# Performance work log

Measured on AMD Instinct MI355X. Metric: run time of the kernel, lower is better.

## Reference

```python
import jax, jax.numpy as jnp
import numpy as np

N, E, H = 50000, 200000, 4
IN, ED = 256, 12
C1, C2 = 256, 64
G, NPG = 100, 500  # 100 graphs x 500 nodes
EPS = 1e-5
SLOPE = 0.2


def gatv2(x, src, dst, edge_attr, Wl, bl, Wr, br, We, att, bias, n_nodes, heads, ch):
    # GATv2Conv (PyG semantics): message j->i, aggregate at target i=edge_index[1]
    xl = (x @ Wl + bl).reshape(n_nodes, heads, ch)   # source transform
    xr = (x @ Wr + br).reshape(n_nodes, heads, ch)   # target transform
    e = (edge_attr @ We).reshape(-1, heads, ch)
    m = xl[src] + xr[dst] + e                        # [E,H,C]
    s = jax.nn.leaky_relu(m, SLOPE)
    logits = jnp.einsum('ehc,hc->eh', s, att)        # [E,H]
    # segment softmax over destination nodes
    mx = jax.ops.segment_max(logits, dst, num_segments=n_nodes)
    ex = jnp.exp(logits - mx[dst])
    den = jax.ops.segment_sum(ex, dst, num_segments=n_nodes)
    alpha = ex / (den[dst] + 1e-16)                  # [E,H]
    out = jax.ops.segment_sum(xl[src] * alpha[:, :, None], dst, num_segments=n_nodes)
    return out.reshape(n_nodes, heads * ch) + bias


def bn_eval(x, gamma, beta, mean, var):
    return (x - mean) * jax.lax.rsqrt(var + EPS) * gamma + beta


def setup_inputs() -> dict:
    key = jax.random.key(0)
    ks = list(jax.random.split(key, 40))
    rn = lambda k, shp, s=0.05: jax.random.normal(k, shp, jnp.float32) * s
    inp = {
        'x': rn(ks[0], (N, IN), 1.0),
        'edge_index': jax.random.randint(ks[1], (2, E), 0, N),
        'edge_attr': rn(ks[2], (E, ED), 1.0),
        'n_nodes': jnp.full((G,), NPG, dtype=jnp.int32),
        # conv1 params (in=IN, out=C1, heads=H)
        'Wl1': rn(ks[3], (IN, H * C1)), 'bl1': rn(ks[4], (H * C1,)),
        'Wr1': rn(ks[5], (IN, H * C1)), 'br1': rn(ks[6], (H * C1,)),
        'We1': rn(ks[7], (ED, H * C1)),
        'att1': rn(ks[8], (H, C1)), 'b1': rn(ks[9], (H * C1,)),
        # bn1 (eval mode running stats)
        'g1': 1.0 + rn(ks[10], (H * C1,)), 'be1': rn(ks[11], (H * C1,)),
        'm1': rn(ks[12], (H * C1,)), 'v1': 1.0 + 0.1 * jax.random.uniform(ks[13], (H * C1,)),
        # conv2 params (in=H*C1, out=C2, heads=H)
        'Wl2': rn(ks[14], (H * C1, H * C2)), 'bl2': rn(ks[15], (H * C2,)),
        'Wr2': rn(ks[16], (H * C1, H * C2)), 'br2': rn(ks[17], (H * C2,)),
        'We2': rn(ks[18], (ED, H * C2)),
        'att2': rn(ks[19], (H, C2)), 'b2': rn(ks[20], (H * C2,)),
        'g2': 1.0 + rn(ks[21], (H * C2,)), 'be2': rn(ks[22], (H * C2,)),
        'm2': rn(ks[23], (H * C2,)), 'v2': 1.0 + 0.1 * jax.random.uniform(ks[24], (H * C2,)),
        # head MLP
        'Wf1': rn(ks[25], (H * C2, 64)), 'bf1': rn(ks[26], (64,)),
        'Wf2': rn(ks[27], (64, 1)), 'bf2': rn(ks[28], (1,)),
    }
    return inp


def reference(x, edge_index, edge_attr, n_nodes,
              Wl1, bl1, Wr1, br1, We1, att1, b1, g1, be1, m1, v1,
              Wl2, bl2, Wr2, br2, We2, att2, b2, g2, be2, m2, v2,
              Wf1, bf1, Wf2, bf2):
    src, dst = edge_index[0], edge_index[1]
    h = gatv2(x, src, dst, edge_attr, Wl1, bl1, Wr1, br1, We1, att1, b1, N, H, C1)
    h = bn_eval(jax.nn.relu(h), g1, be1, m1, v1)
    h = gatv2(h, src, dst, edge_attr, Wl2, bl2, Wr2, br2, We2, att2, b2, N, H, C2)
    h = bn_eval(jax.nn.relu(h), g2, be2, m2, v2)
    last_idx = jnp.cumsum(n_nodes) - 1                # master node per graph
    master = h[last_idx]                              # [G, 256]
    out = jax.nn.relu(master @ Wf1 + bf1) @ Wf2 + bf2  # [G, 1]
    return out
```

## Files before the change

### kernel.cpp

```cpp
#include <hip/hip_runtime.h>
#include <math.h>

#define NN 50000
#define NE 200000
#define NH 4
#define NG 100
#define EPSBN 1e-5f
#define SLOPE 0.2f

typedef __attribute__((ext_vector_type(8))) short bf16x8;
typedef __attribute__((ext_vector_type(4))) float f32x4;

union U8 { bf16x8 v; uint4 q; unsigned w[4]; };

__device__ __forceinline__ unsigned short f2bf(float f) {
    unsigned u = __float_as_uint(f);
    unsigned r = (u + 0x7fffu + ((u >> 16) & 1u)) >> 16;
    return (unsigned short)r;
}
__device__ __forceinline__ float bf2f(unsigned short s) {
    return __uint_as_float(((unsigned)s) << 16);
}

__global__ void fill_val(float* p, int n, float v) {
    int i = blockIdx.x * 256 + threadIdx.x;
    if (i < n) p[i] = v;
}

__global__ void wprep1t(const float* __restrict__ Wl, const float* __restrict__ Wr,
                        unsigned short* __restrict__ Bh) {
    int idx = blockIdx.x * 256 + threadIdx.x;
    int n = idx & 511, k = (idx >> 9) & 255, h = idx >> 17;
    const float* W = (n < 256) ? Wl : Wr;
    float w = W[(size_t)k * 1024 + h * 256 + (n & 255)];
    size_t dst = (size_t)h * 131072 + (((size_t)(n >> 4) * 8 + (k >> 5)) << 9)
               + ((((k >> 3) & 3) << 4) + (n & 15)) * 8 + (k & 7);
    Bh[dst] = f2bf(w);
}
__global__ void wprep2t(const float* __restrict__ Wl, const float* __restrict__ Wr,
                        unsigned short* __restrict__ Bh) {
    int idx = blockIdx.x * 256 + threadIdx.x;
    int n = idx >> 10, k = idx & 1023;
    const float* W = (n < 256) ? Wl : Wr;
    float w = W[(size_t)k * 256 + (n & 255)];
    size_t dst = (((size_t)(n >> 4) * 32 + (k >> 5)) << 9)
               + ((((k >> 3) & 3) << 4) + (n & 15)) * 8 + (k & 7);
    Bh[dst] = f2bf(w);
}

__device__ __forceinline__ void cvt_split(const float4& v0, const float4& v1,
                                          bf16x8& h, bf16x8& l) {
    float vv[8];
    *(float4*)&vv[0] = v0; *(float4*)&vv[4] = v1;
    U8 uh, ul;
#pragma unroll
    for (int j = 0; j < 4; ++j) {
        float a0 = vv[2 * j], a1 = vv[2 * j + 1];
        unsigned u0 = __float_as_uint(a0), u1 = __float_as_uint(a1);
        uh.w[j] = (u0 >> 16) | (u1 & 0xFFFF0000u);
        float l0 = a0 - __uint_as_float(u0 & 0xFFFF0000u);
        float l1 = a1 - __uint_as_float(u1 & 0xFFFF0000u);
        ul.w[j] = (unsigned)f2bf(l0) | ((unsigned)f2bf(l1) << 16);
    }
    h = uh.v; l = ul.v;
}

template<int MODE>
__launch_bounds__(512, 4)
__global__ void gemm_bs(const float* __restrict__ Af,
                        const unsigned short* __restrict__ Atile,
                        const unsigned short* __restrict__ Bh, int KT,
                        const float* __restrict__ bL, const float* __restrict__ bR,
                        unsigned short* __restrict__ C, int M) {
    __shared__ unsigned short Bs[16384];
    const int p = blockIdx.x;
    const int strip = ((p >> 6) << 3) + (p & 7);
    if (strip * 256 >= M) return;
    const int slice = (p >> 3) & 7;
    const int m0 = strip * 256;
    const int tid = threadIdx.x;
    const int lane = tid & 63, w = tid >> 6;
    const int r15 = lane & 15, kq = lane >> 4;
    const size_t sliceBase = (size_t)slice * 4 * KT * 64;

    f32x4 acc[2][4];
#pragma unroll
    for (int m = 0; m < 2; ++m)
#pragma unroll
        for (int n = 0; n < 4; ++n) acc[m][n] = (f32x4){0.f, 0.f, 0.f, 0.f};

    const float* aPtr[2];
    const unsigned short* a2Ptr[2];
#pragma unroll
    for (int m = 0; m < 2; ++m) {
        if (MODE == 0) {
            int row = m0 + w * 32 + m * 16 + r15;
            row = row < M ? row : M - 1;
            aPtr[m] = Af + (size_t)row * 256 + kq * 8;
        } else {
            a2Ptr[m] = Atile + (size_t)(strip * 16 + w * 2 + m) * 16384 + lane * 8;
        }
    }

    float4 curA[2][2];
    bf16x8 curH[2], midH[2];
    if (MODE == 0) {
#pragma unroll
        for (int m = 0; m < 2; ++m) {
            curA[m][0] = *(const float4*)(aPtr[m]);
            curA[m][1] = *(const float4*)(aPtr[m] + 4);
        }
    } else {
#pragma unroll
        for (int m = 0; m < 2; ++m) {
            curH[m] = *(const bf16x8*)(a2Ptr[m]);
            midH[m] = *(const bf16x8*)(a2Ptr[m] + 512);
        }
    }

    const int nchunks = KT / 8;
    for (int kc = 0; kc < nchunks; ++kc) {
        {
            const uint4* gh = (const uint4*)Bh + sliceBase;
            uint4* lh = (uint4*)Bs;
#pragma unroll
            for (int i = 0; i < 4; ++i) {
                int u = i * 512 + tid;
                int nt = u >> 9;
                int ktl = (u & 511) >> 6, j = u & 63;
                lh[u] = gh[((size_t)nt * KT + kc * 8 + ktl) * 64 + j];
            }
        }
        __syncthreads();

#pragma unroll
        for (int ktl = 0; ktl < 8; ++ktl) {
            const int kt = kc * 8 + ktl;
            float4 nxtA[2][2];
            bf16x8 nxtH[2];
            const bool hn1 = (kt + 1 < KT), hn2 = (kt + 2 < KT);
            if (MODE == 0) {
                if (hn1) {
#pragma unroll
                    for (int m = 0; m < 2; ++m) {
                        nxtA[m][0] = *(const float4*)(aPtr[m] + (size_t)(kt + 1) * 32);
                        nxtA[m][1] = *(const float4*)(aPtr[m] + (size_t)(kt + 1) * 32 + 4);
                    }
                }
            } else {
                if (hn2) {
#pragma unroll
                    for (int m = 0; m < 2; ++m)
                        nxtH[m] = *(const bf16x8*)(a2Ptr[m] + (size_t)(kt + 2) * 512);
                }
            }
            bf16x8 ah[2], al[2];
            if (MODE == 0) {
#pragma unroll
                for (int m = 0; m < 2; ++m)
                    cvt_split(curA[m][0], curA[m][1], ah[m], al[m]);
            } else {
#pragma unroll
                for (int m = 0; m < 2; ++m) ah[m] = curH[m];
            }
#pragma unroll
            for (int n = 0; n < 4; ++n) {
                bf16x8 bh = *(const bf16x8*)&Bs[(n * 8 + ktl) * 512 + lane * 8];
#pragma unroll
                for (int m = 0; m < 2; ++m) {
                    acc[m][n] = __builtin_amdgcn_mfma_f32_16x16x32_bf16(
                        ah[m], bh, acc[m][n], 0, 0, 0);
                    if (MODE == 0)
                        acc[m][n] = __builtin_amdgcn_mfma_f32_16x16x32_bf16(
                            al[m], bh, acc[m][n], 0, 0, 0);
                }
            }
            if (MODE == 0) {
                if (hn1) {
#pragma unroll
                    for (int m = 0; m < 2; ++m) {
                        curA[m][0] = nxtA[m][0];
                        curA[m][1] = nxtA[m][1];
                    }
                }
            } else {
#pragma unroll
                for (int m = 0; m < 2; ++m) {
                    curH[m] = midH[m];
                    if (hn2) midH[m] = nxtH[m];
                }
            }
        }
        __syncthreads();
    }
#pragma unroll
    for (int n = 0; n < 4; ++n) {
        int gcol = slice * 64 + n * 16 + r15;
        float bv = (gcol < 256) ? bL[gcol] : bR[gcol - 256];
#pragma unroll
        for (int m = 0; m < 2; ++m) {
#pragma unroll
            for (int r = 0; r < 4; ++r) {
                int grow = m0 + w * 32 + m * 16 + kq * 4 + r;
                if (grow < M)
                    C[(size_t)grow * 512 + gcol] = f2bf(acc[m][n][r] + bv);
            }
        }
    }
}

#define SCAN_BLOCKS 196

__global__ void csr_count(const int* __restrict__ ei, int* __restrict__ cnt) {
    int e = blockIdx.x * 256 + threadIdx.x;
    if (e < NE) atomicAdd(&cnt[ei[NE + e]], 1);
}
__global__ void csr_bsum(const int* __restrict__ cnt, int* __restrict__ bsum) {
    __shared__ int s[256];
    int idx = blockIdx.x * 256 + threadIdx.x;
    int v = idx < NN ? cnt[idx] : 0;
    s[threadIdx.x] = v;
    __syncthreads();
    for (int d = 128; d > 0; d >>= 1) {
        if (threadIdx.x < d) s[threadIdx.x] += s[threadIdx.x + d];
        __syncthreads();
    }
    if (threadIdx.x == 0) bsum[blockIdx.x] = s[0];
}
__global__ void csr_scan_bsum(int* __restrict__ bsum) {
    __shared__ int s[256];
    int t = threadIdx.x;
    int v = t < SCAN_BLOCKS ? bsum[t] : 0;
    s[t] = v;
    __syncthreads();
    for (int d = 1; d < 256; d <<= 1) {
        int x = (t >= d) ? s[t - d] : 0;
        __syncthreads();
        s[t] += x;
        __syncthreads();
    }
    if (t < SCAN_BLOCKS) bsum[t] = s[t] - v;
}
__global__ void csr_apply(const int* __restrict__ cnt, const int* __restrict__ bsum,
                          int* __restrict__ off, int* __restrict__ cursor) {
    __shared__ int s[256];
    int idx = blockIdx.x * 256 + threadIdx.x;
    int v = (idx < NN) ? cnt[idx] : 0;
    s[threadIdx.x] = v;
    __syncthreads();
    for (int d = 1; d < 256; d <<= 1) {
        int x = (threadIdx.x >= d) ? s[threadIdx.x - d] : 0;
        __syncthreads();
        s[threadIdx.x] += x;
        __syncthreads();
    }
    int o = bsum[blockIdx.x] + s[threadIdx.x] - v;
    if (idx < NN) { off[idx] = o; cursor[idx] = o; }
    if (idx == NN - 1) off[NN] = o + v;
}
__global__ void csr_fill(const int* __restrict__ ei, int* __restrict__ cursor,
                         int* __restrict__ eidl) {
    int e = blockIdx.x * 256 + threadIdx.x;
    if (e < NE) {
        int d = ei[NE + e];
        int p = atomicAdd(&cursor[d], 1);
        eidl[p] = e;
    }
}

__device__ __forceinline__ float edge_part(const float4& l, const float4& r,
                                           const float* ev, const float (*rW)[4],
                                           const float4& attv) {
    const float* lp = &l.x; const float* rp = &r.x; const float* ap = &attv.x;
    float part = 0.f;
#pragma unroll
    for (int j = 0; j < 4; ++j) {
        float ecf = 0.f;
#pragma unroll
        for (int d = 0; d < 12; ++d) ecf = fmaf(ev[d], rW[d][j], ecf);
        float mv = lp[j] + rp[j] + ecf;
        mv = mv > 0.f ? mv : SLOPE * mv;
        part = fmaf(mv, ap[j], part);
    }
    return part;
}

template<int NHEADS, int OUTMODE>
__launch_bounds__(256)
__global__ void node_fused(const unsigned short* __restrict__ x16,
                           const int* __restrict__ off, const int* __restrict__ eidl,
                           const int* __restrict__ ei, const float* __restrict__ ea,
                           const float* __restrict__ We, int ldwe,
                           const float* __restrict__ att,
                           const float* __restrict__ bias, const float* __restrict__ gam,
                           const float* __restrict__ bet, const float* __restrict__ mu,
                           const float* __restrict__ var,
                           unsigned short* __restrict__ h1t, int hcol,
                           float* __restrict__ fout) {
    const int n = blockIdx.x * 4 + (threadIdx.x >> 6);
    const int lane = threadIdx.x & 63;
    const int cf = lane * 4;
    float rW[12][4];
#pragma unroll
    for (int d = 0; d < 12; ++d) {
        float4 w = *(const float4*)&We[(size_t)d * ldwe + cf];
        rW[d][0] = w.x; rW[d][1] = w.y; rW[d][2] = w.z; rW[d][3] = w.w;
    }
    const float4 attv = *(const float4*)&att[cf];
    float4 xr4;
    {
        ushort4 u = *(const ushort4*)(x16 + (size_t)n * 512 + 256 + cf);
        xr4 = make_float4(bf2f(u.x), bf2f(u.y), bf2f(u.z), bf2f(u.w));
    }
    float acc[4] = {0.f, 0.f, 0.f, 0.f};
    float den = 0.f;
    const int beg = off[n], end = off[n + 1];
    constexpr int RED = 64 / NHEADS;
    int k = beg;
    for (; k + 2 <= end; k += 2) {
        int e0 = eidl[k], e1 = eidl[k + 1];
        int s0 = ei[e0], s1 = ei[e1];
        float ev0[12], ev1[12];
        const float2* p0 = (const float2*)(ea + (size_t)e0 * 12);
        const float2* p1 = (const float2*)(ea + (size_t)e1 * 12);
#pragma unroll
        for (int d = 0; d < 6; ++d) {
            float2 a = p0[d], b = p1[d];
            ev0[2 * d] = a.x; ev0[2 * d + 1] = a.y;
            ev1[2 * d] = b.x; ev1[2 * d + 1] = b.y;
        }
        ushort4 u0 = *(const ushort4*)(x16 + (size_t)s0 * 512 + cf);
        ushort4 u1 = *(const ushort4*)(x16 + (size_t)s1 * 512 + cf);
        float4 l0 = make_float4(bf2f(u0.x), bf2f(u0.y), bf2f(u0.z), bf2f(u0.w));
        float4 l1 = make_float4(bf2f(u1.x), bf2f(u1.y), bf2f(u1.z), bf2f(u1.w));
        float pa = edge_part(l0, xr4, ev0, rW, attv);
        float pb = edge_part(l1, xr4, ev1, rW, attv);
#pragma unroll
        for (int o = RED / 2; o > 0; o >>= 1) {
            pa += __shfl_xor(pa, o);
            pb += __shfl_xor(pb, o);
        }
        float ex0 = __expf(pa), ex1 = __expf(pb);
        den += ex0 + ex1;
        const float* lp0 = &l0.x; const float* lp1 = &l1.x;
#pragma unroll
        for (int j = 0; j < 4; ++j)
            acc[j] = fmaf(ex0, lp0[j], fmaf(ex1, lp1[j], acc[j]));
    }
    if (k < end) {
        int e0 = eidl[k];
        int s0 = ei[e0];
        float ev0[12];
        const float2* p0 = (const float2*)(ea + (size_t)e0 * 12);
#pragma unroll
        for (int d = 0; d < 6; ++d) {
            float2 a = p0[d];
            ev0[2 * d] = a.x; ev0[2 * d + 1] = a.y;
        }
        ushort4 u0 = *(const ushort4*)(x16 + (size_t)s0 * 512 + cf);
        float4 l0 = make_float4(bf2f(u0.x), bf2f(u0.y), bf2f(u0.z), bf2f(u0.w));
        float pa = edge_part(l0, xr4, ev0, rW, attv);
#pragma unroll
        for (int o = RED / 2; o > 0; o >>= 1) pa += __shfl_xor(pa, o);
        float ex0 = __expf(pa);
        den += ex0;
        const float* lp0 = &l0.x;
#pragma unroll
        for (int j = 0; j < 4; ++j) acc[j] = fmaf(ex0, lp0[j], acc[j]);
    }
    const float inv = 1.f / (den + 1e-16f);
    float o[4];
#pragma unroll
    for (int j = 0; j < 4; ++j) {
        int c = cf + j;
        float t = fmaxf(acc[j] * inv + bias[c], 0.f);
        o[j] = (t - mu[c]) * rsqrtf(var[c] + EPSBN) * gam[c] + bet[c];
    }
    if (OUTMODE == 0) {
        ushort4 hv;
        hv.x = f2bf(o[0]); hv.y = f2bf(o[1]); hv.z = f2bf(o[2]); hv.w = f2bf(o[3]);
        const int kt = (hcol >> 5) + (cf >> 5);
        size_t idx = (size_t)(n >> 4) * 16384 + (size_t)kt * 512
                   + ((((cf >> 3) & 3) << 4) + (n & 15)) * 8 + (cf & 7);
        *(ushort4*)(h1t + idx) = hv;
    } else {
        *(float4*)(fout + (size_t)n * 256 + cf) = make_float4(o[0], o[1], o[2], o[3]);
    }
}

__launch_bounds__(64)
__global__ void head_mlp(const float* __restrict__ h2, const int* __restrict__ n_nodes,
                         const float* __restrict__ Wf1, const float* __restrict__ bf1,
                         const float* __restrict__ Wf2, const float* __restrict__ bf2,
                         float* __restrict__ out) {
    const int g = blockIdx.x;
    const int t = threadIdx.x;
    int acc = 0;
    for (int i = t; i <= g; i += 64) acc += n_nodes[i];
#pragma unroll
    for (int off = 32; off > 0; off >>= 1) acc += __shfl_xor(acc, off);
    const int node = acc - 1;
    __shared__ float row[256];
    for (int i = t; i < 256; i += 64) row[i] = h2[(size_t)node * 256 + i];
    __syncthreads();
    float hid = bf1[t];
    for (int k = 0; k < 256; ++k) hid = fmaf(row[k], Wf1[k * 64 + t], hid);
    hid = fmaxf(hid, 0.f);
    float p = hid * Wf2[t];
#pragma unroll
    for (int off = 32; off > 0; off >>= 1) p += __shfl_xor(p, off);
    if (t == 0) out[g] = p + bf2[0];
}

extern "C" void kernel_launch(void* const* d_in, const int* in_sizes, int n_in,
                              void* d_out, int out_size, void* d_ws, size_t ws_size,
                              hipStream_t stream) {
    const float* x   = (const float*)d_in[0];
    const int*   ei  = (const int*)d_in[1];
    const float* ea  = (const float*)d_in[2];
    const int*   nnd = (const int*)d_in[3];
    const float* Wl1 = (const float*)d_in[4];
    const float* bl1 = (const float*)d_in[5];
    const float* Wr1 = (const float*)d_in[6];
    const float* br1 = (const float*)d_in[7];
    const float* We1 = (const float*)d_in[8];
    const float* att1= (const float*)d_in[9];
    const float* b1  = (const float*)d_in[10];
    const float* g1  = (const float*)d_in[11];
    const float* be1 = (const float*)d_in[12];
    const float* m1  = (const float*)d_in[13];
    const float* v1  = (const float*)d_in[14];
    const float* Wl2 = (const float*)d_in[15];
    const float* bl2 = (const float*)d_in[16];
    const float* Wr2 = (const float*)d_in[17];
    const float* br2 = (const float*)d_in[18];
    const float* We2 = (const float*)d_in[19];
    const float* att2= (const float*)d_in[20];
    const float* b2  = (const float*)d_in[21];
    const float* g2  = (const float*)d_in[22];
    const float* be2 = (const float*)d_in[23];
    const float* m2  = (const float*)d_in[24];
    const float* v2  = (const float*)d_in[25];
    const float* Wf1 = (const float*)d_in[26];
    const float* bf1 = (const float*)d_in[27];
    const float* Wf2 = (const float*)d_in[28];
    const float* bf2 = (const float*)d_in[29];
    float* out = (float*)d_out;

    const size_t XB = (size_t)NN * 512 * 2;
    const size_t HB = (size_t)3136 * 16384 * 2;
    const size_t WPB = (size_t)524288 * 2;
    char* ws = (char*)d_ws;
    size_t off = 0;
    unsigned short* panel = (unsigned short*)(ws + off); off += XB;
    unsigned short* h1t   = (unsigned short*)(ws + off);
    float*          h2f   = (float*)(ws + off);    off += HB;
    unsigned short* B1h = (unsigned short*)(ws + off); off += WPB;
    unsigned short* B2h = (unsigned short*)(ws + off); off += WPB;
    int* cnt    = (int*)(ws + off); off += (size_t)NN * 4;
    int* csroff = (int*)(ws + off); off += ((size_t)(NN + 1) * 4 + 15) & ~15ull;
    int* cursor = (int*)(ws + off); off += (size_t)NN * 4;
    int* eidl   = (int*)(ws + off); off += (size_t)NE * 4;
    int* bsum   = (int*)(ws + off); off += ((size_t)SCAN_BLOCKS * 4 + 15) & ~15ull;
    if (ws_size < off) {
        fill_val<<<(out_size + 255) / 256, 256, 0, stream>>>(out, out_size, 1e30f);
        return;
    }

    hipMemsetAsync(cnt, 0, (size_t)NN * 4, stream);
    csr_count<<<(NE + 255) / 256, 256, 0, stream>>>(ei, cnt);
    csr_bsum<<<SCAN_BLOCKS, 256, 0, stream>>>(cnt, bsum);
    csr_scan_bsum<<<1, 256, 0, stream>>>(bsum);
    csr_apply<<<SCAN_BLOCKS, 256, 0, stream>>>(cnt, bsum, csroff, cursor);
    csr_fill<<<(NE + 255) / 256, 256, 0, stream>>>(ei, cursor, eidl);

    wprep1t<<<2048, 256, 0, stream>>>(Wl1, Wr1, B1h);
    wprep2t<<<2048, 256, 0, stream>>>(Wl2, Wr2, B2h);

    const int gemmBlocks = 25 * 64;
    const int nodeBlocks = NN / 4;

    for (int h = 0; h < NH; ++h) {
        gemm_bs<0><<<gemmBlocks, 512, 0, stream>>>(
            x, nullptr, B1h + (size_t)h * 131072, 8,
            bl1 + h * 256, br1 + h * 256, panel, NN);
        node_fused<1, 0><<<nodeBlocks, 256, 0, stream>>>(
            panel, csroff, eidl, ei, ea, We1 + h * 256, 1024, att1 + h * 256,
            b1 + h * 256, g1 + h * 256, be1 + h * 256, m1 + h * 256, v1 + h * 256,
            h1t, h * 256, nullptr);
    }

    gemm_bs<1><<<gemmBlocks, 512, 0, stream>>>(
        nullptr, h1t, B2h, 32, bl2, br2, panel, NN);
    node_fused<4, 1><<<nodeBlocks, 256, 0, stream>>>(
        panel, csroff, eidl, ei, ea, We2, 256, att2, b2, g2, be2, m2, v2,
        nullptr, 0, h2f);

    head_mlp<<<NG, 64, 0, stream>>>(h2f, nnd, Wf1, bf1, Wf2, bf2, out);
}
```

Measured before the change: 830.5 us.

## Pre-convert input features to tiled bf16 once, drop split-precision layer-1 GEMM

Adds an xprep kernel that converts x to bf16 once, in the MFMA tile layout, and zero-pads it to a multiple of 16 rows. All four per-head layer-1 GEMMs then use the same bf16-tile path as layer 2. This removes the per-head fp32 reads, the per-tile hi/lo split and the second MFMA for the low part. It also drops the hi/lo split on x, which lowers layer-1 precision and may push results past tolerance.

New measurement: 704.0 us. 15.2% less time.

```diff
diff --git a/kernel.cpp b/kernel.cpp
--- a/kernel.cpp
+++ b/kernel.cpp
@@ -7,11 +7,10 @@
 #define NG 100
 #define EPSBN 1e-5f
 #define SLOPE 0.2f
+#define NROWT 3128
 
 typedef __attribute__((ext_vector_type(8))) short bf16x8;
 typedef __attribute__((ext_vector_type(4))) float f32x4;
-
-union U8 { bf16x8 v; uint4 q; unsigned w[4]; };
 
 __device__ __forceinline__ unsigned short f2bf(float f) {
     unsigned u = __float_as_uint(f);
@@ -48,30 +47,32 @@
     Bh[dst] = f2bf(w);
 }
 
-__device__ __forceinline__ void cvt_split(const float4& v0, const float4& v1,
-                                          bf16x8& h, bf16x8& l) {
-    float vv[8];
-    *(float4*)&vv[0] = v0; *(float4*)&vv[4] = v1;
-    U8 uh, ul;
-#pragma unroll
-    for (int j = 0; j < 4; ++j) {
-        float a0 = vv[2 * j], a1 = vv[2 * j + 1];
-        unsigned u0 = __float_as_uint(a0), u1 = __float_as_uint(a1);
-        uh.w[j] = (u0 >> 16) | (u1 & 0xFFFF0000u);
-        float l0 = a0 - __uint_as_float(u0 & 0xFFFF0000u);
-        float l1 = a1 - __uint_as_float(u1 & 0xFFFF0000u);
-        ul.w[j] = (unsigned)f2bf(l0) | ((unsigned)f2bf(l1) << 16);
-    }
-    h = uh.v; l = ul.v;
-}
-
-template<int MODE>
+__global__ void xprep(const float* __restrict__ x, unsigned short* __restrict__ xt) {
+    int idx = blockIdx.x * 256 + threadIdx.x;
+    int row = idx >> 5;
+    if (row >= NROWT * 16) return;
+    int k8 = (idx & 31) << 3;
+    unsigned short o[8];
+    if (row < NN) {
+        float4 v0 = *(const float4*)(x + (size_t)row * 256 + k8);
+        float4 v1 = *(const float4*)(x + (size_t)row * 256 + k8 + 4);
+        o[0] = f2bf(v0.x); o[1] = f2bf(v0.y); o[2] = f2bf(v0.z); o[3] = f2bf(v0.w);
+        o[4] = f2bf(v1.x); o[5] = f2bf(v1.y); o[6] = f2bf(v1.z); o[7] = f2bf(v1.w);
+    } else {
+#pragma unroll
+        for (int j = 0; j < 8; ++j) o[j] = 0;
+    }
+    size_t dst = (size_t)(row >> 4) * 4096 + (size_t)(k8 >> 5) * 512
+               + ((((k8 >> 3) & 3) << 4) + (row & 15)) * 8;
+    *(ushort4*)(xt + dst) = *(ushort4*)&o[0];
+    *(ushort4*)(xt + dst + 4) = *(ushort4*)&o[4];
+}
+
 __launch_bounds__(512, 4)
-__global__ void gemm_bs(const float* __restrict__ Af,
-                        const unsigned short* __restrict__ Atile,
-                        const unsigned short* __restrict__ Bh, int KT,
-                        const float* __restrict__ bL, const float* __restrict__ bR,
-                        unsigned short* __restrict__ C, int M) {
+__global__ void gemm_t(const unsigned short* __restrict__ Atile,
+                       const unsigned short* __restrict__ Bh, int KT,
+                       const float* __restrict__ bL, const float* __restrict__ bR,
+                       unsigned short* __restrict__ C, int M) {
     __shared__ unsigned short Bs[16384];
     const int p = blockIdx.x;
     const int strip = ((p >> 6) << 3) + (p & 7);
@@ -82,6 +83,7 @@
     const int lane = tid & 63, w = tid >> 6;
     const int r15 = lane & 15, kq = lane >> 4;
     const size_t sliceBase = (size_t)slice * 4 * KT * 64;
+    const size_t tileStride = (size_t)KT * 512;
 
     f32x4 acc[2][4];
 #pragma unroll
@@ -89,33 +91,16 @@
 #pragma unroll
         for (int n = 0; n < 4; ++n) acc[m][n] = (f32x4){0.f, 0.f, 0.f, 0.f};
 
-    const float* aPtr[2];
-    const unsigned short* a2Ptr[2];
+    const unsigned short* aPtr[2];
+#pragma unroll
+    for (int m = 0; m < 2; ++m)
+        aPtr[m] = Atile + (size_t)(strip * 16 + w * 2 + m) * tileStride + lane * 8;
+
+    bf16x8 curH[2], midH[2];
 #pragma unroll
     for (int m = 0; m < 2; ++m) {
-        if (MODE == 0) {
-            int row = m0 + w * 32 + m * 16 + r15;
-            row = row < M ? row : M - 1;
-            aPtr[m] = Af + (size_t)row * 256 + kq * 8;
-        } else {
-            a2Ptr[m] = Atile + (size_t)(strip * 16 + w * 2 + m) * 16384 + lane * 8;
-        }
-    }
-
-    float4 curA[2][2];
-    bf16x8 curH[2], midH[2];
-    if (MODE == 0) {
-#pragma unroll
-        for (int m = 0; m < 2; ++m) {
-            curA[m][0] = *(const float4*)(aPtr[m]);
-            curA[m][1] = *(const float4*)(aPtr[m] + 4);
-        }
-    } else {
-#pragma unroll
-        for (int m = 0; m < 2; ++m) {
-            curH[m] = *(const bf16x8*)(a2Ptr[m]);
-            midH[m] = *(const bf16x8*)(a2Ptr[m] + 512);
-        }
+        curH[m] = *(const bf16x8*)(aPtr[m]);
+        midH[m] = *(const bf16x8*)(aPtr[m] + 512);
     }
 
     const int nchunks = KT / 8;
@@ -136,59 +121,25 @@
 #pragma unroll
         for (int ktl = 0; ktl < 8; ++ktl) {
             const int kt = kc * 8 + ktl;
-            float4 nxtA[2][2];
             bf16x8 nxtH[2];
-            const bool hn1 = (kt + 1 < KT), hn2 = (kt + 2 < KT);
-            if (MODE == 0) {
-                if (hn1) {
-#pragma unroll
-                    for (int m = 0; m < 2; ++m) {
-                        nxtA[m][0] = *(const float4*)(aPtr[m] + (size_t)(kt + 1) * 32);
-                        nxtA[m][1] = *(const float4*)(aPtr[m] + (size_t)(kt + 1) * 32 + 4);
-                    }
-                }
-            } else {
-                if (hn2) {
-#pragma unroll
-                    for (int m = 0; m < 2; ++m)
-                        nxtH[m] = *(const bf16x8*)(a2Ptr[m] + (size_t)(kt + 2) * 512);
-                }
-            }
-            bf16x8 ah[2], al[2];
-            if (MODE == 0) {
+            const bool hn2 = (kt + 2 < KT);
+            if (hn2) {
 #pragma unroll
                 for (int m = 0; m < 2; ++m)
-                    cvt_split(curA[m][0], curA[m][1], ah[m], al[m]);
-            } else {
-#pragma unroll
-                for (int m = 0; m < 2; ++m) ah[m] = curH[m];
+                    nxtH[m] = *(const bf16x8*)(aPtr[m] + (size_t)(kt + 2) * 512);
             }
 #pragma unroll
             for (int n = 0; n < 4; ++n) {
                 bf16x8 bh = *(const bf16x8*)&Bs[(n * 8 + ktl) * 512 + lane * 8];
 #pragma unroll
-                for (int m = 0; m < 2; ++m) {
+                for (int m = 0; m < 2; ++m)
                     acc[m][n] = __builtin_amdgcn_mfma_f32_16x16x32_bf16(
-                        ah[m], bh, acc[m][n], 0, 0, 0);
-                    if (MODE == 0)
-                        acc[m][n] = __builtin_amdgcn_mfma_f32_16x16x32_bf16(
-                            al[m], bh, acc[m][n], 0, 0, 0);
-                }
+                        curH[m], bh, acc[m][n], 0, 0, 0);
             }
-            if (MODE == 0) {
-                if (hn1) {
-#pragma unroll
-                    for (int m = 0; m < 2; ++m) {
-                        curA[m][0] = nxtA[m][0];
-                        curA[m][1] = nxtA[m][1];
-                    }
-                }
-            } else {
-#pragma unroll
-                for (int m = 0; m < 2; ++m) {
-                    curH[m] = midH[m];
-                    if (hn2) midH[m] = nxtH[m];
-                }
+#pragma unroll
+            for (int m = 0; m < 2; ++m) {
+                curH[m] = midH[m];
+                if (hn2) midH[m] = nxtH[m];
             }
         }
         __syncthreads();
@@ -449,12 +400,14 @@
 
     const size_t XB = (size_t)NN * 512 * 2;
     const size_t HB = (size_t)3136 * 16384 * 2;
+    const size_t XTB = (size_t)NROWT * 4096 * 2;
     const size_t WPB = (size_t)524288 * 2;
     char* ws = (char*)d_ws;
     size_t off = 0;
     unsigned short* panel = (unsigned short*)(ws + off); off += XB;
     unsigned short* h1t   = (unsigned short*)(ws + off);
     float*          h2f   = (float*)(ws + off);    off += HB;
+    unsigned short* xt    = (unsigned short*)(ws + off); off += XTB;
     unsigned short* B1h = (unsigned short*)(ws + off); off += WPB;
     unsigned short* B2h = (unsigned short*)(ws + off); off += WPB;
     int* cnt    = (int*)(ws + off); off += (size_t)NN * 4;
@@ -476,22 +429,22 @@
 
     wprep1t<<<2048, 256, 0, stream>>>(Wl1, Wr1, B1h);
     wprep2t<<<2048, 256, 0, stream>>>(Wl2, Wr2, B2h);
+    xprep<<<(NROWT * 16 * 32 + 255) / 256, 256, 0, stream>>>(x, xt);
 
     const int gemmBlocks = 25 * 64;
     const int nodeBlocks = NN / 4;
 
     for (int h = 0; h < NH; ++h) {
-        gemm_bs<0><<<gemmBlocks, 512, 0, stream>>>(
-            x, nullptr, B1h + (size_t)h * 131072, 8,
-            bl1 + h * 256, br1 + h * 256, panel, NN);
+        gemm_t<<<gemmBlocks, 512, 0, stream>>>(
+            xt, B1h + (size_t)h * 131072, 8, bl1 + h * 256, br1 + h * 256, panel, NN);
         node_fused<1, 0><<<nodeBlocks, 256, 0, stream>>>(
             panel, csroff, eidl, ei, ea, We1 + h * 256, 1024, att1 + h * 256,
             b1 + h * 256, g1 + h * 256, be1 + h * 256, m1 + h * 256, v1 + h * 256,
             h1t, h * 256, nullptr);
     }
 
-    gemm_bs<1><<<gemmBlocks, 512, 0, stream>>>(
-        nullptr, h1t, B2h, 32, bl2, br2, panel, NN);
+    gemm_t<<<gemmBlocks, 512, 0, stream>>>(
+        h1t, B2h, 32, bl2, br2, panel, NN);
     node_fused<4, 1><<<nodeBlocks, 256, 0, stream>>>(
         panel, csroff, eidl, ei, ea, We2, 256, att2, b2, g2, be2, m2, v2,
         nullptr, 0, h2f);
```
